# Kernel tuning notes

Hardware: AMD Instinct MI355X
Metric: run time of the kernel (lower is better)

The kernel has to match this reference:

```python
import jax, jax.numpy as jnp
import numpy as np

N, IN_FEAT, OUT_FEAT = 16384, 1024, 4096


def setup_inputs() -> dict:
    key = jax.random.key(0)
    k_x, k_m, k_w, k_b = jax.random.split(key, 4)
    x = jax.random.normal(k_x, (N, IN_FEAT), dtype=jnp.float32)
    amask = jax.random.randint(k_m, (N,), 0, 2, dtype=jnp.int32)
    # nn.Linear(in_feat, out_feat): weight [out, in], bias [out]
    W = jax.random.normal(k_w, (OUT_FEAT, IN_FEAT), dtype=jnp.float32) * (1.0 / np.sqrt(IN_FEAT))
    b = jax.random.normal(k_b, (OUT_FEAT,), dtype=jnp.float32) * 0.001
    return {"x": x, "amask": amask, "W": W, "b": b}


def reference(x, amask, W, b):
    # Torch code gathers rows where amask != 0, applies linear (+identity act),
    # and scatters results back into a zero [N, out_feat] tensor. Equivalent
    # dense-math (jit-friendly, no data-dependent shapes): compute the linear
    # on all rows and zero out unmasked rows. Same output values.
    y = jnp.einsum('ni,oi->no', x, W) + b  # [N, out_feat]
    keep = (amask != 0)[:, None]
    return jnp.where(keep, y, jnp.zeros((), dtype=x.dtype))
```

## Files before the change

kernel.cpp:

```cpp
#include <hip/hip_runtime.h>
#include <hip/hip_bf16.h>
#include <stdint.h>

#define N_ROWS 16384
#define K_DIM  1024
#define N_OUT  4096

typedef __attribute__((ext_vector_type(8))) short short8;
typedef __attribute__((ext_vector_type(4))) float f32x4;
typedef __attribute__((ext_vector_type(4))) __bf16 bf16x4;

__global__ __launch_bounds__(1024) void scan_kernel(const int* __restrict__ amask,
                                                    int* __restrict__ idx,
                                                    int* __restrict__ zidx,
                                                    int* __restrict__ count) {
    __shared__ int sc[1024];
    const int t = threadIdx.x;
    const int base = t * 16;
    int mk[16];
#pragma unroll
    for (int g = 0; g < 4; ++g) {
        int4 m4 = reinterpret_cast<const int4*>(amask + base)[g];
        mk[g*4+0] = m4.x; mk[g*4+1] = m4.y; mk[g*4+2] = m4.z; mk[g*4+3] = m4.w;
    }
    int c = 0;
#pragma unroll
    for (int i = 0; i < 16; ++i) c += (mk[i] != 0) ? 1 : 0;
    int v = c;
    sc[t] = v;
    __syncthreads();
    for (int off = 1; off < 1024; off <<= 1) {
        int u = (t >= off) ? sc[t - off] : 0;
        __syncthreads();
        v += u; sc[t] = v;
        __syncthreads();
    }
    int b  = v - c;
    int zb = base - b;
#pragma unroll
    for (int i = 0; i < 16; ++i) {
        int r = base + i;
        if (mk[i] != 0) idx[b++] = r; else zidx[zb++] = r;
    }
    if (t == 1023) count[0] = v;
}

__global__ __launch_bounds__(256) void cvtw_gather_kernel(
    const float* __restrict__ W, const float* __restrict__ x,
    const int* __restrict__ idx, const int* __restrict__ count,
    __bf16* __restrict__ wb, __bf16* __restrict__ xb) {
    const int t = threadIdx.x;
    if (blockIdx.x < 256) {
        const int base = blockIdx.x * 4096 + t;
#pragma unroll
        for (int it = 0; it < 16; ++it) {
            const int i = base + it * 256;
            float4 v = reinterpret_cast<const float4*>(W)[i];
            bf16x4 o;
            o[0] = (__bf16)v.x; o[1] = (__bf16)v.y; o[2] = (__bf16)v.z; o[3] = (__bf16)v.w;
            reinterpret_cast<bf16x4*>(wb)[i] = o;
        }
        return;
    }
    const int cnt = count[0];
    for (int j = blockIdx.x - 256; j < cnt; j += 2048) {
        const int row = idx[j];
        float4 v = reinterpret_cast<const float4*>(x + (size_t)row * K_DIM)[t];
        bf16x4 o;
        o[0] = (__bf16)v.x; o[1] = (__bf16)v.y; o[2] = (__bf16)v.z; o[3] = (__bf16)v.w;
        reinterpret_cast<bf16x4*>(xb + (size_t)j * K_DIM)[t] = o;
    }
}


#define GLL(SRC, DSTOFF)                                                       \
    __builtin_amdgcn_global_load_lds(                                          \
        (const __attribute__((address_space(1))) void*)(SRC),                  \
        (__attribute__((address_space(3))) void*)(ldsc + (DSTOFF)), 16, 0, 0)

__global__ __launch_bounds__(256) void gemm_kernel(
    const __bf16* __restrict__ A,
    const __bf16* __restrict__ B,
    const float*  __restrict__ bias,
    const int*    __restrict__ idx,
    const int*    __restrict__ zidx,
    const int*    __restrict__ count,
    float*        __restrict__ out)
{
    __shared__ short lds_all[8192];

    const int cnt = count[0];
    const int aT  = (cnt + 127) >> 7;
    const int tn  = blockIdx.x & 31;
    const int tm  = blockIdx.x >> 5;
    const int t   = threadIdx.x;
    const int nz  = N_ROWS - cnt;
    const float4 zf = make_float4(0.f, 0.f, 0.f, 0.f);

    if (tm >= aT) {
        if (aT == 0) {
            for (int i = blockIdx.x; i < nz; i += 4096) {
                const int row = zidx[i];
                float4* p = reinterpret_cast<float4*>(out + (size_t)row * N_OUT);
#pragma unroll
                for (int u = 0; u < 4; ++u)
                    p[u * 256 + t] = zf;
            }
        }
        return;
    }

    const int l  = t & 63;
    const int w  = t >> 6;
    const int wm = w >> 1;
    const int wn = w & 1;

    const int m0 = tm * 128;
    const int n0 = tn * 128;

    const int srow = t >> 2;
    const int sk8  = (t & 3) * 8;
    const __bf16* pA0 = A + (size_t)(m0 + srow) * K_DIM + sk8;
    const __bf16* pA1 = pA0 + (size_t)64 * K_DIM;
    const __bf16* pB0 = B + (size_t)(n0 + srow) * K_DIM + sk8;
    const __bf16* pB1 = pB0 + (size_t)64 * K_DIM;
    char* ldsc = (char*)lds_all;

    const int lr = l & 15;
    const int lk = (l >> 4) * 8;

    f32x4 acc[4][4] = {};

    for (int k0 = 0; k0 < K_DIM; k0 += 32) {
        GLL(pA0 + k0, t * 16);
        GLL(pA1 + k0, 4096 + t * 16);
        GLL(pB0 + k0, 8192 + t * 16);
        GLL(pB1 + k0, 12288 + t * 16);
        __syncthreads();

        short8 af[4], bf[4];
#pragma unroll
        for (int mi = 0; mi < 4; ++mi)
            af[mi] = *(const short8*)(lds_all + (wm*64 + mi*16 + lr)*32 + lk);
#pragma unroll
        for (int ni = 0; ni < 4; ++ni)
            bf[ni] = *(const short8*)(lds_all + 4096 + (wn*64 + ni*16 + lr)*32 + lk);

#pragma unroll
        for (int mi = 0; mi < 4; ++mi)
#pragma unroll
            for (int ni = 0; ni < 4; ++ni)
                acc[mi][ni] = __builtin_amdgcn_mfma_f32_16x16x32_bf16(
                    af[mi], bf[ni], acc[mi][ni], 0, 0, 0);
        __syncthreads();
    }

    const int lq = l >> 4;
    float bv[4];
#pragma unroll
    for (int ni = 0; ni < 4; ++ni) bv[ni] = bias[n0 + wn*64 + ni*16 + lr];

#pragma unroll
    for (int mi = 0; mi < 4; ++mi) {
        const int slot0 = m0 + wm*64 + mi*16 + lq*4;
        int rowid[4]; bool val[4];
#pragma unroll
        for (int r = 0; r < 4; ++r) {
            const int s = slot0 + r;
            val[r] = (s < cnt);
            rowid[r] = val[r] ? idx[s] : 0;
        }
#pragma unroll
        for (int ni = 0; ni < 4; ++ni) {
            const int cc = n0 + wn*64 + ni*16 + lr;
#pragma unroll
            for (int r = 0; r < 4; ++r)
                if (val[r]) out[(size_t)rowid[r] * N_OUT + cc] = acc[mi][ni][r] + bv[ni];
        }
    }

    const int nheavy = aT * 32;
    for (int i = blockIdx.x; i < nz; i += nheavy) {
        const int row = zidx[i];
        float4* p = reinterpret_cast<float4*>(out + (size_t)row * N_OUT);
#pragma unroll
        for (int u = 0; u < 4; ++u)
            p[u * 256 + t] = zf;
    }
}

__global__ void naive_kernel(const float* __restrict__ x, const float* __restrict__ W,
                             const float* __restrict__ bias, const int* __restrict__ amask,
                             float* __restrict__ out) {
    int c = blockIdx.x * blockDim.x + threadIdx.x;
    int r = blockIdx.y;
    if (c >= N_OUT) return;
    if (amask[r] == 0) { out[(size_t)r * N_OUT + c] = 0.0f; return; }
    const float* xr = x + (size_t)r * K_DIM;
    const float* wr = W + (size_t)c * K_DIM;
    float s = 0.0f;
    for (int k = 0; k < K_DIM; ++k) s += xr[k] * wr[k];
    out[(size_t)r * N_OUT + c] = s + bias[c];
}

extern "C" void kernel_launch(void* const* d_in, const int* in_sizes, int n_in,
                              void* d_out, int out_size, void* d_ws, size_t ws_size,
                              hipStream_t stream) {
    const float* x     = (const float*)d_in[0];
    const int*   amask = (const int*)d_in[1];
    const float* W     = (const float*)d_in[2];
    const float* bias  = (const float*)d_in[3];
    float*       out   = (float*)d_out;

    const size_t xb_bytes = (size_t)N_ROWS * K_DIM * 2;
    const size_t wb_bytes = (size_t)N_OUT  * K_DIM * 2;
    const size_t idx_bytes = (size_t)N_ROWS * 4;
    const size_t need = xb_bytes + wb_bytes + 2 * idx_bytes + 256;

    if (ws_size < need) {
        dim3 g((N_OUT + 255) / 256, N_ROWS);
        naive_kernel<<<g, 256, 0, stream>>>(x, W, bias, amask, out);
        return;
    }

    __bf16* xb   = (__bf16*)d_ws;
    __bf16* wb   = (__bf16*)((char*)d_ws + xb_bytes);
    int*    idx  = (int*)((char*)d_ws + xb_bytes + wb_bytes);
    int*    zidx = idx + N_ROWS;
    int*    cnt  = zidx + N_ROWS;

    scan_kernel<<<1, 1024, 0, stream>>>(amask, idx, zidx, cnt);
    cvtw_gather_kernel<<<2304, 256, 0, stream>>>(W, x, idx, cnt, wb, xb);
    gemm_kernel<<<4096, 256, 0, stream>>>(xb, wb, bias, idx, zidx, cnt, out);
}
```

Baseline: 153.7 us.

## Stage GEMM epilogue through LDS for coalesced float4 scatter; move zero-fill to idle blocks

The epilogue now writes accumulators into LDS in four 32-row chunks, then each thread writes contiguous float4 segments of whole output rows with bias added. This replaces scattered per-element 4-byte stores with 512-byte coalesced row writes. Zero-filling of masked-out rows moves from the heavy GEMM blocks to the otherwise idle blocks beyond the active tile range, so GEMM blocks no longer do that tail work. The cost is extra LDS traffic and barriers in the epilogue.

```diff
diff --git a/kernel.cpp b/kernel.cpp
--- a/kernel.cpp
+++ b/kernel.cpp
@@ -94,18 +94,18 @@
     const int tn  = blockIdx.x & 31;
     const int tm  = blockIdx.x >> 5;
     const int t   = threadIdx.x;
-    const int nz  = N_ROWS - cnt;
-    const float4 zf = make_float4(0.f, 0.f, 0.f, 0.f);
 
     if (tm >= aT) {
-        if (aT == 0) {
-            for (int i = blockIdx.x; i < nz; i += 4096) {
-                const int row = zidx[i];
-                float4* p = reinterpret_cast<float4*>(out + (size_t)row * N_OUT);
-#pragma unroll
-                for (int u = 0; u < 4; ++u)
-                    p[u * 256 + t] = zf;
-            }
+        const int ntriv = 4096 - aT * 32;
+        const int tr    = blockIdx.x - aT * 32;
+        const int nz    = N_ROWS - cnt;
+        const float4 zf = make_float4(0.f, 0.f, 0.f, 0.f);
+        for (int i = tr; i < nz; i += ntriv) {
+            const int row = zidx[i];
+            float4* p = reinterpret_cast<float4*>(out + (size_t)row * N_OUT);
+#pragma unroll
+            for (int u = 0; u < 4; ++u)
+                p[u * 256 + t] = zf;
         }
         return;
     }
@@ -128,6 +128,7 @@
 
     const int lr = l & 15;
     const int lk = (l >> 4) * 8;
+    const int lq = l >> 4;
 
     f32x4 acc[4][4] = {};
 
@@ -155,37 +156,37 @@
         __syncthreads();
     }
 
-    const int lq = l >> 4;
-    float bv[4];
-#pragma unroll
-    for (int ni = 0; ni < 4; ++ni) bv[ni] = bias[n0 + wn*64 + ni*16 + lr];
-
-#pragma unroll
-    for (int mi = 0; mi < 4; ++mi) {
-        const int slot0 = m0 + wm*64 + mi*16 + lq*4;
-        int rowid[4]; bool val[4];
-#pragma unroll
-        for (int r = 0; r < 4; ++r) {
-            const int s = slot0 + r;
-            val[r] = (s < cnt);
-            rowid[r] = val[r] ? idx[s] : 0;
-        }
-#pragma unroll
-        for (int ni = 0; ni < 4; ++ni) {
-            const int cc = n0 + wn*64 + ni*16 + lr;
-#pragma unroll
-            for (int r = 0; r < 4; ++r)
-                if (val[r]) out[(size_t)rowid[r] * N_OUT + cc] = acc[mi][ni][r] + bv[ni];
-        }
-    }
-
-    const int nheavy = aT * 32;
-    for (int i = blockIdx.x; i < nz; i += nheavy) {
-        const int row = zidx[i];
-        float4* p = reinterpret_cast<float4*>(out + (size_t)row * N_OUT);
-#pragma unroll
-        for (int u = 0; u < 4; ++u)
-            p[u * 256 + t] = zf;
+    float* eps = reinterpret_cast<float*>(lds_all);
+    const int lcol  = l & 31;
+    const int lhalf = l >> 5;
+    const float4 bias4 = *reinterpret_cast<const float4*>(bias + n0 + lcol * 4);
+
+#pragma unroll
+    for (int q = 0; q < 4; ++q) {
+        const int mi0 = (q & 1) * 2;
+        if (wm == (q >> 1)) {
+#pragma unroll
+            for (int mm = 0; mm < 2; ++mm)
+#pragma unroll
+                for (int ni = 0; ni < 4; ++ni)
+#pragma unroll
+                    for (int r = 0; r < 4; ++r)
+                        eps[(mm*16 + lq*4 + r)*128 + wn*64 + ni*16 + lr] =
+                            acc[mi0 + mm][ni][r];
+        }
+        __syncthreads();
+#pragma unroll
+        for (int rr = 0; rr < 4; ++rr) {
+            const int lrow = w*8 + rr*2 + lhalf;
+            const int s = m0 + q*32 + lrow;
+            if (s < cnt) {
+                const int row = idx[s];
+                float4 v = *reinterpret_cast<const float4*>(&eps[lrow*128 + lcol*4]);
+                v.x += bias4.x; v.y += bias4.y; v.z += bias4.z; v.w += bias4.w;
+                *reinterpret_cast<float4*>(out + (size_t)row * N_OUT + n0 + lcol*4) = v;
+            }
+        }
+        __syncthreads();
     }
 }
 
```

After: 179.2 us. 16.6% more time.
